# Optimization experiments

Measured on AMD Instinct MI355X. Metric: run time of the kernel, lower is better.

## Reference

```python
import jax, jax.numpy as jnp
import numpy as np

S, N, CM, CZ, H, C = 256, 512, 256, 128, 8, 32
EPS = 1e-5


def layer_norm(x, gamma, beta):
    mu = jnp.mean(x, axis=-1, keepdims=True)
    var = jnp.var(x, axis=-1, keepdims=True)
    return (x - mu) * jax.lax.rsqrt(var + EPS) * gamma + beta


def setup_inputs() -> dict:
    key = jax.random.key(0)
    ks = jax.random.split(key, 10)
    sc = lambda fan_in: 1.0 / np.sqrt(fan_in)
    return {
        "msa_rep": jax.random.normal(ks[0], (S, N, CM), dtype=jnp.float32),
        "pair_rep": jax.random.normal(ks[1], (N, N, CZ), dtype=jnp.float32),
        "ln_msa_g": jnp.ones((CM,), jnp.float32),
        "ln_msa_b": jnp.zeros((CM,), jnp.float32),
        "Wv": jax.random.uniform(ks[2], (CM, H * C), jnp.float32, -sc(CM), sc(CM)),
        "bv": jax.random.uniform(ks[3], (H * C,), jnp.float32, -sc(CM), sc(CM)),
        "ln_z_g": jnp.ones((CZ,), jnp.float32),
        "ln_z_b": jnp.zeros((CZ,), jnp.float32),
        "Wb": jax.random.uniform(ks[4], (CZ, H), jnp.float32, -sc(CZ), sc(CZ)),
        "bb": jax.random.uniform(ks[5], (H,), jnp.float32, -sc(CZ), sc(CZ)),
        "Wg": jax.random.uniform(ks[6], (CM, H * C), jnp.float32, -sc(CM), sc(CM)),
        "bg": jax.random.uniform(ks[7], (H * C,), jnp.float32, -sc(CM), sc(CM)),
        "Wp": jax.random.uniform(ks[8], (H * C, CM), jnp.float32, -sc(H * C), sc(H * C)),
    }


def reference(msa_rep, pair_rep, ln_msa_g, ln_msa_b, Wv, bv, ln_z_g, ln_z_b, Wb, bb, Wg, bg, Wp):
    m = layer_norm(msa_rep, ln_msa_g, ln_msa_b)                 # [S,N,CM]
    v = (m @ Wv + bv).reshape(S, N, H, C)                       # [S,N,H,C]
    g = jax.nn.sigmoid(m @ Wg + bg).reshape(S, N, H, C)         # [S,N,H,C]
    b = layer_norm(pair_rep, ln_z_g, ln_z_b) @ Wb + bb          # [N,N,H]
    w = jax.nn.softmax(b, axis=-2)                              # softmax over key residue j
    # o[s,i,h,c] = sum_j w[i,j,h] * v[s,j,h,c]
    o = g * jnp.einsum('ijh,sjhc->sihc', w, v)                  # [S,N,H,C]
    return o.reshape(S, N, H * C) @ Wp                          # [S,N,CM]
```

## Files before the change

### kernel.cpp

```cpp
#include <hip/hip_runtime.h>
#include <hip/hip_bf16.h>
#include <math.h>

#define S 256
#define N 512
#define CM 256
#define CZ 128
#define H 8
#define C 32
#define HC 256

typedef __attribute__((ext_vector_type(8))) short short8v;
typedef __attribute__((ext_vector_type(4))) float f32x4;

#define GLOBAL_LOAD_LDS16(gsrc, ldst)                                          \
  __builtin_amdgcn_global_load_lds(                                            \
      (const __attribute__((address_space(1))) void*)(gsrc),                   \
      (__attribute__((address_space(3))) void*)(ldst), 16, 0, 0)

__global__ __launch_bounds__(256) void k_prep(
    const float* __restrict__ Wv, const float* __restrict__ Wg, const float* __restrict__ Wp,
    __hip_bfloat16* __restrict__ Wcat_t, __hip_bfloat16* __restrict__ Wp_t)
{
  const int k = blockIdx.x;
  const int n = threadIdx.x;
  Wcat_t[(size_t)n * CM + k]        = __float2bfloat16(Wv[(size_t)k * HC + n]);
  Wcat_t[(size_t)(n + HC) * CM + k] = __float2bfloat16(Wg[(size_t)k * HC + n]);
  Wp_t[(size_t)n * CM + k]          = __float2bfloat16(Wp[(size_t)k * CM + n]);
}

__global__ __launch_bounds__(256) void k_ln(
    const float* __restrict__ msa, const float* __restrict__ gamma, const float* __restrict__ beta,
    __hip_bfloat16* __restrict__ mbf)
{
  const int t = threadIdx.x, wav = t >> 6, lane = t & 63;
  const size_t row = (size_t)blockIdx.x * 4 + wav;
  const int k0 = lane * 4;
  const float4 xv = *(const float4*)(msa + row * CM + k0);
  float s  = xv.x + xv.y + xv.z + xv.w;
  float s2 = xv.x * xv.x + xv.y * xv.y + xv.z * xv.z + xv.w * xv.w;
#pragma unroll
  for (int off = 32; off > 0; off >>= 1) {
    s  += __shfl_xor(s, off);
    s2 += __shfl_xor(s2, off);
  }
  const float mu = s * (1.f / CM);
  const float rstd = rsqrtf(s2 * (1.f / CM) - mu * mu + 1e-5f);
  const float4 gm = *(const float4*)(gamma + k0);
  const float4 bt = *(const float4*)(beta + k0);
  union { __hip_bfloat16 b[4]; short4 v; } pk;
  pk.b[0] = __float2bfloat16((xv.x - mu) * rstd * gm.x + bt.x);
  pk.b[1] = __float2bfloat16((xv.y - mu) * rstd * gm.y + bt.y);
  pk.b[2] = __float2bfloat16((xv.z - mu) * rstd * gm.z + bt.z);
  pk.b[3] = __float2bfloat16((xv.w - mu) * rstd * gm.w + bt.w);
  *(short4*)(mbf + row * CM + k0) = pk.v;
}

__global__ __launch_bounds__(256) void k_mm1(
    const __hip_bfloat16* __restrict__ mbf, const __hip_bfloat16* __restrict__ Wcat_t,
    const float* __restrict__ bv, const float* __restrict__ bg,
    __hip_bfloat16* __restrict__ vc, __hip_bfloat16* __restrict__ gb)
{
  __shared__ __hip_bfloat16 Ac[8 * 128 * 8];
  __shared__ __hip_bfloat16 Bc[8 * 128 * 8];
  const int t = threadIdx.x;
  const int wave = t >> 6, lane = t & 63;
  const int wm = wave >> 1, wn = wave & 1;
  const int lr = lane & 15, lq = lane >> 4;
  const int n0 = blockIdx.x * 128;
  const int m0 = blockIdx.y * 128;

  float bias[4];
#pragma unroll
  for (int ni = 0; ni < 4; ++ni) {
    const int col = n0 + wn * 64 + ni * 16 + lr;
    bias[ni] = (col < HC) ? bv[col] : bg[col - HC];
  }
  f32x4 acc[4][4];
#pragma unroll
  for (int mi = 0; mi < 4; ++mi)
#pragma unroll
    for (int ni = 0; ni < 4; ++ni) acc[mi][ni] = (f32x4)bias[ni];

  for (int kt = 0; kt < CM / 64; ++kt) {
    __syncthreads();
#pragma unroll
    for (int u = 0; u < 2; ++u) {
      const int jb = wave * 2 + u;
#pragma unroll
      for (int ih = 0; ih < 2; ++ih) {
        const __hip_bfloat16* asrc = mbf + ((size_t)(m0 + ih * 64 + lane)) * CM + kt * 64 + jb * 8;
        GLOBAL_LOAD_LDS16(asrc, &Ac[(jb * 128 + ih * 64) * 8]);
        const __hip_bfloat16* bsrc = Wcat_t + ((size_t)(n0 + ih * 64 + lane)) * CM + kt * 64 + jb * 8;
        GLOBAL_LOAD_LDS16(bsrc, &Bc[(jb * 128 + ih * 64) * 8]);
      }
    }
    __syncthreads();
#pragma unroll
    for (int kh = 0; kh < 2; ++kh) {
      const int ldb = lq + kh * 4;
      short8v a[4], b[4];
#pragma unroll
      for (int mi = 0; mi < 4; ++mi)
        a[mi] = *(const short8v*)&Ac[((ldb * 128) + wm * 64 + mi * 16 + lr) * 8];
#pragma unroll
      for (int ni = 0; ni < 4; ++ni)
        b[ni] = *(const short8v*)&Bc[((ldb * 128) + wn * 64 + ni * 16 + lr) * 8];
#pragma unroll
      for (int mi = 0; mi < 4; ++mi)
#pragma unroll
        for (int ni = 0; ni < 4; ++ni)
          acc[mi][ni] = __builtin_amdgcn_mfma_f32_16x16x32_bf16(a[mi], b[ni], acc[mi][ni], 0, 0, 0);
    }
  }

  if (n0 < HC) {
#pragma unroll
    for (int mi = 0; mi < 4; ++mi) {
      const int rowb = m0 + wm * 64 + mi * 16 + lq * 4;
      const int s = rowb >> 9;
      const int j = rowb & (N - 1);
      const int jb = j >> 3, jlo = (lq & 1) * 4;
#pragma unroll
      for (int ni = 0; ni < 4; ++ni) {
        const int col = n0 + wn * 64 + ni * 16 + lr;
        const int h = col >> 5, c = col & 31;
        union { __hip_bfloat16 b[4]; short4 v; } pk;
#pragma unroll
        for (int r = 0; r < 4; ++r) pk.b[r] = __float2bfloat16(acc[mi][ni][r]);
        *(short4*)(vc + ((size_t)(h * (N / 8) + jb) * (S * C) + s * C + c) * 8 + jlo) = pk.v;
      }
    }
  } else {
#pragma unroll
    for (int mi = 0; mi < 4; ++mi) {
      const int rowb = m0 + wm * 64 + mi * 16 + lq * 4;
#pragma unroll
      for (int ni = 0; ni < 4; ++ni) {
        const int colp = (n0 - HC) + wn * 64 + ni * 16 + lr;
#pragma unroll
        for (int r = 0; r < 4; ++r)
          gb[(size_t)(rowb + r) * HC + colp] =
              __float2bfloat16(1.f / (1.f + __expf(-acc[mi][ni][r])));
      }
    }
  }
}

__global__ __launch_bounds__(256) void k_ln_b(
    const float* __restrict__ pair, const float* __restrict__ gamma, const float* __restrict__ beta,
    const float* __restrict__ Wb, float* __restrict__ wbuf)
{
  const int t = threadIdx.x, wav = t >> 6, lane = t & 63;
  const int q = lane & 15, sub = lane >> 4;
  const int k0 = q * 8;

  float wreg[8][8];
#pragma unroll
  for (int kk = 0; kk < 8; ++kk) {
    *(float4*)&wreg[kk][0] = *(const float4*)&Wb[(k0 + kk) * H];
    *(float4*)&wreg[kk][4] = *(const float4*)&Wb[(k0 + kk) * H + 4];
  }
  const float4 gm0 = *(const float4*)(gamma + k0);
  const float4 gm1 = *(const float4*)(gamma + k0 + 4);
  const float4 bt0 = *(const float4*)(beta + k0);
  const float4 bt1 = *(const float4*)(beta + k0 + 4);

#pragma unroll 2
  for (int it = 0; it < 8; ++it) {
    const size_t row = (size_t)blockIdx.x * 128 + it * 16 + wav * 4 + sub;
    const float* x = pair + row * CZ + k0;
    const float4 x0 = *(const float4*)(x);
    const float4 x1 = *(const float4*)(x + 4);

    float s  = x0.x + x0.y + x0.z + x0.w + x1.x + x1.y + x1.z + x1.w;
    float s2 = x0.x * x0.x + x0.y * x0.y + x0.z * x0.z + x0.w * x0.w
             + x1.x * x1.x + x1.y * x1.y + x1.z * x1.z + x1.w * x1.w;
#pragma unroll
    for (int off = 8; off > 0; off >>= 1) {
      s  += __shfl_xor(s, off);
      s2 += __shfl_xor(s2, off);
    }
    const float mu = s * (1.f / CZ);
    const float rstd = rsqrtf(s2 * (1.f / CZ) - mu * mu + 1e-5f);

    float xn[8];
    xn[0] = (x0.x - mu) * rstd * gm0.x + bt0.x;
    xn[1] = (x0.y - mu) * rstd * gm0.y + bt0.y;
    xn[2] = (x0.z - mu) * rstd * gm0.z + bt0.z;
    xn[3] = (x0.w - mu) * rstd * gm0.w + bt0.w;
    xn[4] = (x1.x - mu) * rstd * gm1.x + bt1.x;
    xn[5] = (x1.y - mu) * rstd * gm1.y + bt1.y;
    xn[6] = (x1.z - mu) * rstd * gm1.z + bt1.z;
    xn[7] = (x1.w - mu) * rstd * gm1.w + bt1.w;

    float acc[8];
#pragma unroll
    for (int h = 0; h < 8; ++h) acc[h] = 0.f;
#pragma unroll
    for (int kk = 0; kk < 8; ++kk)
#pragma unroll
      for (int h = 0; h < 8; ++h) acc[h] += xn[kk] * wreg[kk][h];

#pragma unroll
    for (int h = 0; h < 8; ++h) {
#pragma unroll
      for (int off = 8; off > 0; off >>= 1) acc[h] += __shfl_xor(acc[h], off);
    }
    if (q == 0) {
      const size_t i = row >> 9;
      const size_t j = row & (N - 1);
#pragma unroll
      for (int h = 0; h < 8; ++h)
        wbuf[((size_t)h * N + i) * N + j] = acc[h];
    }
  }
}

__global__ __launch_bounds__(256) void k_softmax(
    const float* __restrict__ wbuf, __hip_bfloat16* __restrict__ wbh)
{
  const float* p = wbuf + (size_t)blockIdx.x * N;
  const int t = threadIdx.x, lane = t & 63, wav = t >> 6;
  float2 xv = *(const float2*)(p + t * 2);
  float mx = fmaxf(xv.x, xv.y);
#pragma unroll
  for (int off = 32; off > 0; off >>= 1) mx = fmaxf(mx, __shfl_xor(mx, off));
  __shared__ float redmax[4];
  __shared__ float redsum[4];
  if (lane == 0) redmax[wav] = mx;
  __syncthreads();
  mx = fmaxf(fmaxf(redmax[0], redmax[1]), fmaxf(redmax[2], redmax[3]));
  const float e0 = __expf(xv.x - mx), e1 = __expf(xv.y - mx);
  float sum = e0 + e1;
#pragma unroll
  for (int off = 32; off > 0; off >>= 1) sum += __shfl_xor(sum, off);
  if (lane == 0) redsum[wav] = sum;
  __syncthreads();
  sum = (redsum[0] + redsum[1]) + (redsum[2] + redsum[3]);
  const float inv = 1.f / sum;
  union { __hip_bfloat16 b[2]; int i; } pk;
  pk.b[0] = __float2bfloat16(e0 * inv);
  pk.b[1] = __float2bfloat16(e1 * inv);
  *(int*)((__hip_bfloat16*)(wbh + (size_t)blockIdx.x * N) + t * 2) = pk.i;
}

__global__ __launch_bounds__(256) void k_attn_mfma(
    const __hip_bfloat16* __restrict__ vc, const __hip_bfloat16* __restrict__ wbh,
    __hip_bfloat16* gb)
{
  __shared__ __hip_bfloat16 Ac[8 * 128 * 8];
  __shared__ __hip_bfloat16 Bc[8 * 128 * 8];

  const int t = threadIdx.x;
  const int wave = t >> 6, lane = t & 63;
  const int wm = wave >> 1, wn = wave & 1;
  const int lr = lane & 15, lq = lane >> 4;
  const int n0 = blockIdx.x * 128;
  const int i0 = blockIdx.y * 128;
  const int h  = blockIdx.z;

  f32x4 acc[4][4];
#pragma unroll
  for (int mi = 0; mi < 4; ++mi)
#pragma unroll
    for (int ni = 0; ni < 4; ++ni) acc[mi][ni] = (f32x4)0.f;

  const __hip_bfloat16* Abase = wbh + ((size_t)h * N + i0) * N;
  const __hip_bfloat16* Bbase = vc + (size_t)h * (N / 8) * (S * C) * 8 + (size_t)n0 * 8;

  for (int kt = 0; kt < N / 64; ++kt) {
    __syncthreads();
#pragma unroll
    for (int u = 0; u < 2; ++u) {
      const int jb = wave * 2 + u;
#pragma unroll
      for (int ih = 0; ih < 2; ++ih) {
        const __hip_bfloat16* asrc = Abase + ((size_t)(ih * 64 + lane)) * N + kt * 64 + jb * 8;
        GLOBAL_LOAD_LDS16(asrc, &Ac[(jb * 128 + ih * 64) * 8]);
        const __hip_bfloat16* bsrc = Bbase + ((size_t)(kt * 8 + jb) * (S * C) + ih * 64 + lane) * 8;
        GLOBAL_LOAD_LDS16(bsrc, &Bc[(jb * 128 + ih * 64) * 8]);
      }
    }
    __syncthreads();

#pragma unroll
    for (int kh = 0; kh < 2; ++kh) {
      const int ldb = lq + kh * 4;
      short8v a[4], b[4];
#pragma unroll
      for (int mi = 0; mi < 4; ++mi)
        a[mi] = *(const short8v*)&Ac[((ldb * 128) + wm * 64 + mi * 16 + lr) * 8];
#pragma unroll
      for (int ni = 0; ni < 4; ++ni)
        b[ni] = *(const short8v*)&Bc[((ldb * 128) + wn * 64 + ni * 16 + lr) * 8];
#pragma unroll
      for (int mi = 0; mi < 4; ++mi)
#pragma unroll
        for (int ni = 0; ni < 4; ++ni)
          acc[mi][ni] = __builtin_amdgcn_mfma_f32_16x16x32_bf16(a[mi], b[ni], acc[mi][ni], 0, 0, 0);
    }
  }

#pragma unroll
  for (int mi = 0; mi < 4; ++mi)
#pragma unroll
    for (int ni = 0; ni < 4; ++ni) {
      const int n = n0 + wn * 64 + ni * 16 + lr;
      const int sidx = n >> 5, c = n & 31;
#pragma unroll
      for (int r = 0; r < 4; ++r) {
        const int i = i0 + wm * 64 + mi * 16 + lq * 4 + r;
        const size_t idx = (((size_t)sidx * N + i) << 8) + h * C + c;
        const float gv = __bfloat162float(gb[idx]);
        gb[idx] = __float2bfloat16(gv * acc[mi][ni][r]);
      }
    }
}

__global__ __launch_bounds__(256) void k_out_mfma(
    const __hip_bfloat16* __restrict__ ogb, const __hip_bfloat16* __restrict__ Wp_t,
    float* __restrict__ out)
{
  __shared__ __hip_bfloat16 Ac[8 * 128 * 8];
  __shared__ __hip_bfloat16 Bc[8 * 128 * 8];
  const int t = threadIdx.x;
  const int wave = t >> 6, lane = t & 63;
  const int wm = wave >> 1, wn = wave & 1;
  const int lr = lane & 15, lq = lane >> 4;
  const int n0 = blockIdx.x * 128;
  const int m0 = blockIdx.y * 128;

  f32x4 acc[4][4];
#pragma unroll
  for (int mi = 0; mi < 4; ++mi)
#pragma unroll
    for (int ni = 0; ni < 4; ++ni) acc[mi][ni] = (f32x4)0.f;

  for (int kt = 0; kt < CM / 64; ++kt) {
    __syncthreads();
#pragma unroll
    for (int u = 0; u < 2; ++u) {
      const int jb = wave * 2 + u;
#pragma unroll
      for (int ih = 0; ih < 2; ++ih) {
        const __hip_bfloat16* asrc = ogb + ((size_t)(m0 + ih * 64 + lane)) * CM + kt * 64 + jb * 8;
        GLOBAL_LOAD_LDS16(asrc, &Ac[(jb * 128 + ih * 64) * 8]);
        const __hip_bfloat16* bsrc = Wp_t + ((size_t)(n0 + ih * 64 + lane)) * CM + kt * 64 + jb * 8;
        GLOBAL_LOAD_LDS16(bsrc, &Bc[(jb * 128 + ih * 64) * 8]);
      }
    }
    __syncthreads();
#pragma unroll
    for (int kh = 0; kh < 2; ++kh) {
      const int ldb = lq + kh * 4;
      short8v a[4], b[4];
#pragma unroll
      for (int mi = 0; mi < 4; ++mi)
        a[mi] = *(const short8v*)&Ac[((ldb * 128) + wm * 64 + mi * 16 + lr) * 8];
#pragma unroll
      for (int ni = 0; ni < 4; ++ni)
        b[ni] = *(const short8v*)&Bc[((ldb * 128) + wn * 64 + ni * 16 + lr) * 8];
#pragma unroll
      for (int mi = 0; mi < 4; ++mi)
#pragma unroll
        for (int ni = 0; ni < 4; ++ni)
          acc[mi][ni] = __builtin_amdgcn_mfma_f32_16x16x32_bf16(a[mi], b[ni], acc[mi][ni], 0, 0, 0);
    }
  }

#pragma unroll
  for (int mi = 0; mi < 4; ++mi) {
    const int rowb = m0 + wm * 64 + mi * 16 + lq * 4;
#pragma unroll
    for (int ni = 0; ni < 4; ++ni) {
      const int col = n0 + wn * 64 + ni * 16 + lr;
#pragma unroll
      for (int r = 0; r < 4; ++r)
        out[(size_t)(rowb + r) * CM + col] = acc[mi][ni][r];
    }
  }
}

extern "C" void kernel_launch(void* const* d_in, const int* in_sizes, int n_in,
                              void* d_out, int out_size, void* d_ws, size_t ws_size,
                              hipStream_t stream)
{
  const float* msa      = (const float*)d_in[0];
  const float* pair     = (const float*)d_in[1];
  const float* ln_msa_g = (const float*)d_in[2];
  const float* ln_msa_b = (const float*)d_in[3];
  const float* Wv       = (const float*)d_in[4];
  const float* bv       = (const float*)d_in[5];
  const float* ln_z_g   = (const float*)d_in[6];
  const float* ln_z_b   = (const float*)d_in[7];
  const float* Wb       = (const float*)d_in[8];
  const float* bb       = (const float*)d_in[9];
  const float* Wg       = (const float*)d_in[10];
  const float* bg       = (const float*)d_in[11];
  const float* Wp       = (const float*)d_in[12];
  float* out = (float*)d_out;
  (void)bb;

  char* w = (char*)d_ws;
  __hip_bfloat16* vc     = (__hip_bfloat16*)(w);
  __hip_bfloat16* mbf    = (__hip_bfloat16*)(w + 67108864);
  __hip_bfloat16* gb     = (__hip_bfloat16*)(w + 134217728);
  float*          wbuf   = (float*)         (w + 201326592);
  __hip_bfloat16* wbh    = (__hip_bfloat16*)(w + 209715200);
  __hip_bfloat16* Wcat_t = (__hip_bfloat16*)(w + 213909504);
  __hip_bfloat16* Wp_t   = (__hip_bfloat16*)(w + 214171648);

  k_prep<<<256, 256, 0, stream>>>(Wv, Wg, Wp, Wcat_t, Wp_t);
  k_ln<<<S * N / 4, 256, 0, stream>>>(msa, ln_msa_g, ln_msa_b, mbf);
  dim3 g1(4, S * N / 128);
  k_mm1<<<g1, 256, 0, stream>>>(mbf, Wcat_t, bv, bg, vc, gb);
  k_ln_b<<<N * N / 128, 256, 0, stream>>>(pair, ln_z_g, ln_z_b, Wb, wbuf);
  k_softmax<<<N * H, 256, 0, stream>>>(wbuf, wbh);
  dim3 g4(S * C / 128, N / 128, H);
  k_attn_mfma<<<g4, 256, 0, stream>>>(vc, wbh, gb);
  dim3 g5(2, S * N / 128);
  k_out_mfma<<<g5, 256, 0, stream>>>(gb, Wp_t, out);
}
```

Baseline: 331.3 us.

## Double-buffer LDS staging in GEMM kernels and transpose MFMA outputs for vector stores

Adds two-stage LDS double buffering to the mm1, attention and output GEMMs, so the next K-tile's global-to-LDS loads are issued before the current tile's MFMAs run. This uses one barrier per iteration instead of two. In the gate half of mm1 and in the attention kernel, the MFMA operands are swapped so each lane holds 4 contiguous columns, which lets the epilogue write packed short4 stores and read-modify-write gb in 4-element chunks instead of scattered 2-byte accesses. The attention grid is reordered so blocks sharing the same V columns (n0) run adjacently, which may improve L2 reuse. LDS usage doubles to 64KB per block, which may reduce occupancy.

```diff
diff --git a/kernel.cpp b/kernel.cpp
--- a/kernel.cpp
+++ b/kernel.cpp
@@ -61,60 +61,83 @@
     const float* __restrict__ bv, const float* __restrict__ bg,
     __hip_bfloat16* __restrict__ vc, __hip_bfloat16* __restrict__ gb)
 {
-  __shared__ __hip_bfloat16 Ac[8 * 128 * 8];
-  __shared__ __hip_bfloat16 Bc[8 * 128 * 8];
+  __shared__ __hip_bfloat16 Ac[2][8 * 128 * 8];
+  __shared__ __hip_bfloat16 Bc[2][8 * 128 * 8];
   const int t = threadIdx.x;
   const int wave = t >> 6, lane = t & 63;
   const int wm = wave >> 1, wn = wave & 1;
   const int lr = lane & 15, lq = lane >> 4;
   const int n0 = blockIdx.x * 128;
   const int m0 = blockIdx.y * 128;
-
-  float bias[4];
-#pragma unroll
-  for (int ni = 0; ni < 4; ++ni) {
-    const int col = n0 + wn * 64 + ni * 16 + lr;
-    bias[ni] = (col < HC) ? bv[col] : bg[col - HC];
-  }
+  const bool vhalf = (n0 < HC);
+
   f32x4 acc[4][4];
-#pragma unroll
-  for (int mi = 0; mi < 4; ++mi)
-#pragma unroll
-    for (int ni = 0; ni < 4; ++ni) acc[mi][ni] = (f32x4)bias[ni];
-
-  for (int kt = 0; kt < CM / 64; ++kt) {
-    __syncthreads();
+  if (vhalf) {
+#pragma unroll
+    for (int ni = 0; ni < 4; ++ni) {
+      const float b_ = bv[n0 + wn * 64 + ni * 16 + lr];
+#pragma unroll
+      for (int mi = 0; mi < 4; ++mi) acc[mi][ni] = (f32x4)b_;
+    }
+  } else {
+#pragma unroll
+    for (int ni = 0; ni < 4; ++ni) {
+      const float4 b4 = *(const float4*)&bg[(n0 - HC) + wn * 64 + ni * 16 + lq * 4];
+#pragma unroll
+      for (int mi = 0; mi < 4; ++mi) {
+        acc[mi][ni][0] = b4.x; acc[mi][ni][1] = b4.y;
+        acc[mi][ni][2] = b4.z; acc[mi][ni][3] = b4.w;
+      }
+    }
+  }
+
+  auto stage = [&](int p, int kt) {
 #pragma unroll
     for (int u = 0; u < 2; ++u) {
       const int jb = wave * 2 + u;
 #pragma unroll
       for (int ih = 0; ih < 2; ++ih) {
-        const __hip_bfloat16* asrc = mbf + ((size_t)(m0 + ih * 64 + lane)) * CM + kt * 64 + jb * 8;
-        GLOBAL_LOAD_LDS16(asrc, &Ac[(jb * 128 + ih * 64) * 8]);
-        const __hip_bfloat16* bsrc = Wcat_t + ((size_t)(n0 + ih * 64 + lane)) * CM + kt * 64 + jb * 8;
-        GLOBAL_LOAD_LDS16(bsrc, &Bc[(jb * 128 + ih * 64) * 8]);
-      }
-    }
-    __syncthreads();
+        GLOBAL_LOAD_LDS16(mbf + ((size_t)(m0 + ih * 64 + lane)) * CM + kt * 64 + jb * 8,
+                          &Ac[p][(jb * 128 + ih * 64) * 8]);
+        GLOBAL_LOAD_LDS16(Wcat_t + ((size_t)(n0 + ih * 64 + lane)) * CM + kt * 64 + jb * 8,
+                          &Bc[p][(jb * 128 + ih * 64) * 8]);
+      }
+    }
+  };
+
+  stage(0, 0);
+  __syncthreads();
+  for (int kt = 0; kt < 4; ++kt) {
+    const int p = kt & 1;
+    if (kt < 3) stage(p ^ 1, kt + 1);
 #pragma unroll
     for (int kh = 0; kh < 2; ++kh) {
       const int ldb = lq + kh * 4;
       short8v a[4], b[4];
 #pragma unroll
       for (int mi = 0; mi < 4; ++mi)
-        a[mi] = *(const short8v*)&Ac[((ldb * 128) + wm * 64 + mi * 16 + lr) * 8];
+        a[mi] = *(const short8v*)&Ac[p][((ldb * 128) + wm * 64 + mi * 16 + lr) * 8];
 #pragma unroll
       for (int ni = 0; ni < 4; ++ni)
-        b[ni] = *(const short8v*)&Bc[((ldb * 128) + wn * 64 + ni * 16 + lr) * 8];
-#pragma unroll
-      for (int mi = 0; mi < 4; ++mi)
-#pragma unroll
-        for (int ni = 0; ni < 4; ++ni)
-          acc[mi][ni] = __builtin_amdgcn_mfma_f32_16x16x32_bf16(a[mi], b[ni], acc[mi][ni], 0, 0, 0);
-    }
-  }
-
-  if (n0 < HC) {
+        b[ni] = *(const short8v*)&Bc[p][((ldb * 128) + wn * 64 + ni * 16 + lr) * 8];
+      if (vhalf) {
+#pragma unroll
+        for (int mi = 0; mi < 4; ++mi)
+#pragma unroll
+          for (int ni = 0; ni < 4; ++ni)
+            acc[mi][ni] = __builtin_amdgcn_mfma_f32_16x16x32_bf16(a[mi], b[ni], acc[mi][ni], 0, 0, 0);
+      } else {
+#pragma unroll
+        for (int mi = 0; mi < 4; ++mi)
+#pragma unroll
+          for (int ni = 0; ni < 4; ++ni)
+            acc[mi][ni] = __builtin_amdgcn_mfma_f32_16x16x32_bf16(b[ni], a[mi], acc[mi][ni], 0, 0, 0);
+      }
+    }
+    __syncthreads();
+  }
+
+  if (vhalf) {
 #pragma unroll
     for (int mi = 0; mi < 4; ++mi) {
       const int rowb = m0 + wm * 64 + mi * 16 + lq * 4;
@@ -134,14 +157,15 @@
   } else {
 #pragma unroll
     for (int mi = 0; mi < 4; ++mi) {
-      const int rowb = m0 + wm * 64 + mi * 16 + lq * 4;
+      const int rowb = m0 + wm * 64 + mi * 16 + lr;
 #pragma unroll
       for (int ni = 0; ni < 4; ++ni) {
-        const int colp = (n0 - HC) + wn * 64 + ni * 16 + lr;
+        const int nb = (n0 - HC) + wn * 64 + ni * 16 + lq * 4;
+        union { __hip_bfloat16 b[4]; short4 v; } pk;
 #pragma unroll
         for (int r = 0; r < 4; ++r)
-          gb[(size_t)(rowb + r) * HC + colp] =
-              __float2bfloat16(1.f / (1.f + __expf(-acc[mi][ni][r])));
+          pk.b[r] = __float2bfloat16(1.f / (1.f + __expf(-acc[mi][ni][r])));
+        *(short4*)(gb + (size_t)rowb * HC + nb) = pk.v;
       }
     }
   }
@@ -249,15 +273,15 @@
     const __hip_bfloat16* __restrict__ vc, const __hip_bfloat16* __restrict__ wbh,
     __hip_bfloat16* gb)
 {
-  __shared__ __hip_bfloat16 Ac[8 * 128 * 8];
-  __shared__ __hip_bfloat16 Bc[8 * 128 * 8];
+  __shared__ __hip_bfloat16 Ac[2][8 * 128 * 8];
+  __shared__ __hip_bfloat16 Bc[2][8 * 128 * 8];
 
   const int t = threadIdx.x;
   const int wave = t >> 6, lane = t & 63;
   const int wm = wave >> 1, wn = wave & 1;
   const int lr = lane & 15, lq = lane >> 4;
-  const int n0 = blockIdx.x * 128;
-  const int i0 = blockIdx.y * 128;
+  const int i0 = blockIdx.x * 128;
+  const int n0 = blockIdx.y * 128;
   const int h  = blockIdx.z;
 
   f32x4 acc[4][4];
@@ -269,61 +293,68 @@
   const __hip_bfloat16* Abase = wbh + ((size_t)h * N + i0) * N;
   const __hip_bfloat16* Bbase = vc + (size_t)h * (N / 8) * (S * C) * 8 + (size_t)n0 * 8;
 
-  for (int kt = 0; kt < N / 64; ++kt) {
-    __syncthreads();
+  auto stage = [&](int p, int kt) {
 #pragma unroll
     for (int u = 0; u < 2; ++u) {
       const int jb = wave * 2 + u;
 #pragma unroll
       for (int ih = 0; ih < 2; ++ih) {
-        const __hip_bfloat16* asrc = Abase + ((size_t)(ih * 64 + lane)) * N + kt * 64 + jb * 8;
-        GLOBAL_LOAD_LDS16(asrc, &Ac[(jb * 128 + ih * 64) * 8]);
-        const __hip_bfloat16* bsrc = Bbase + ((size_t)(kt * 8 + jb) * (S * C) + ih * 64 + lane) * 8;
-        GLOBAL_LOAD_LDS16(bsrc, &Bc[(jb * 128 + ih * 64) * 8]);
-      }
-    }
-    __syncthreads();
-
+        GLOBAL_LOAD_LDS16(Abase + ((size_t)(ih * 64 + lane)) * N + kt * 64 + jb * 8,
+                          &Ac[p][(jb * 128 + ih * 64) * 8]);
+        GLOBAL_LOAD_LDS16(Bbase + ((size_t)(kt * 8 + jb) * (S * C) + ih * 64 + lane) * 8,
+                          &Bc[p][(jb * 128 + ih * 64) * 8]);
+      }
+    }
+  };
+
+  stage(0, 0);
+  __syncthreads();
+  for (int kt = 0; kt < 8; ++kt) {
+    const int p = kt & 1;
+    if (kt < 7) stage(p ^ 1, kt + 1);
 #pragma unroll
     for (int kh = 0; kh < 2; ++kh) {
       const int ldb = lq + kh * 4;
       short8v a[4], b[4];
 #pragma unroll
       for (int mi = 0; mi < 4; ++mi)
-        a[mi] = *(const short8v*)&Ac[((ldb * 128) + wm * 64 + mi * 16 + lr) * 8];
+        a[mi] = *(const short8v*)&Ac[p][((ldb * 128) + wm * 64 + mi * 16 + lr) * 8];
 #pragma unroll
       for (int ni = 0; ni < 4; ++ni)
-        b[ni] = *(const short8v*)&Bc[((ldb * 128) + wn * 64 + ni * 16 + lr) * 8];
+        b[ni] = *(const short8v*)&Bc[p][((ldb * 128) + wn * 64 + ni * 16 + lr) * 8];
 #pragma unroll
       for (int mi = 0; mi < 4; ++mi)
 #pragma unroll
         for (int ni = 0; ni < 4; ++ni)
-          acc[mi][ni] = __builtin_amdgcn_mfma_f32_16x16x32_bf16(a[mi], b[ni], acc[mi][ni], 0, 0, 0);
-    }
-  }
-
-#pragma unroll
-  for (int mi = 0; mi < 4; ++mi)
+          acc[mi][ni] = __builtin_amdgcn_mfma_f32_16x16x32_bf16(b[ni], a[mi], acc[mi][ni], 0, 0, 0);
+    }
+    __syncthreads();
+  }
+
+#pragma unroll
+  for (int mi = 0; mi < 4; ++mi) {
+    const int i = i0 + wm * 64 + mi * 16 + lr;
 #pragma unroll
     for (int ni = 0; ni < 4; ++ni) {
-      const int n = n0 + wn * 64 + ni * 16 + lr;
-      const int sidx = n >> 5, c = n & 31;
-#pragma unroll
-      for (int r = 0; r < 4; ++r) {
-        const int i = i0 + wm * 64 + mi * 16 + lq * 4 + r;
-        const size_t idx = (((size_t)sidx * N + i) << 8) + h * C + c;
-        const float gv = __bfloat162float(gb[idx]);
-        gb[idx] = __float2bfloat16(gv * acc[mi][ni][r]);
-      }
-    }
+      const int nb = n0 + wn * 64 + ni * 16 + lq * 4;
+      const int sidx = nb >> 5, c = nb & 31;
+      __hip_bfloat16* gp = gb + (((size_t)sidx * N + i) << 8) + h * C + c;
+      union { __hip_bfloat16 b[4]; short4 v; } gl, st;
+      gl.v = *(const short4*)gp;
+#pragma unroll
+      for (int r = 0; r < 4; ++r)
+        st.b[r] = __float2bfloat16(__bfloat162float(gl.b[r]) * acc[mi][ni][r]);
+      *(short4*)gp = st.v;
+    }
+  }
 }
 
 __global__ __launch_bounds__(256) void k_out_mfma(
     const __hip_bfloat16* __restrict__ ogb, const __hip_bfloat16* __restrict__ Wp_t,
     float* __restrict__ out)
 {
-  __shared__ __hip_bfloat16 Ac[8 * 128 * 8];
-  __shared__ __hip_bfloat16 Bc[8 * 128 * 8];
+  __shared__ __hip_bfloat16 Ac[2][8 * 128 * 8];
+  __shared__ __hip_bfloat16 Bc[2][8 * 128 * 8];
   const int t = threadIdx.x;
   const int wave = t >> 6, lane = t & 63;
   const int wm = wave >> 1, wn = wave & 1;
@@ -337,36 +368,42 @@
 #pragma unroll
     for (int ni = 0; ni < 4; ++ni) acc[mi][ni] = (f32x4)0.f;
 
-  for (int kt = 0; kt < CM / 64; ++kt) {
-    __syncthreads();
+  auto stage = [&](int p, int kt) {
 #pragma unroll
     for (int u = 0; u < 2; ++u) {
       const int jb = wave * 2 + u;
 #pragma unroll
       for (int ih = 0; ih < 2; ++ih) {
-        const __hip_bfloat16* asrc = ogb + ((size_t)(m0 + ih * 64 + lane)) * CM + kt * 64 + jb * 8;
-        GLOBAL_LOAD_LDS16(asrc, &Ac[(jb * 128 + ih * 64) * 8]);
-        const __hip_bfloat16* bsrc = Wp_t + ((size_t)(n0 + ih * 64 + lane)) * CM + kt * 64 + jb * 8;
-        GLOBAL_LOAD_LDS16(bsrc, &Bc[(jb * 128 + ih * 64) * 8]);
-      }
-    }
-    __syncthreads();
+        GLOBAL_LOAD_LDS16(ogb + ((size_t)(m0 + ih * 64 + lane)) * CM + kt * 64 + jb * 8,
+                          &Ac[p][(jb * 128 + ih * 64) * 8]);
+        GLOBAL_LOAD_LDS16(Wp_t + ((size_t)(n0 + ih * 64 + lane)) * CM + kt * 64 + jb * 8,
+                          &Bc[p][(jb * 128 + ih * 64) * 8]);
+      }
+    }
+  };
+
+  stage(0, 0);
+  __syncthreads();
+  for (int kt = 0; kt < 4; ++kt) {
+    const int p = kt & 1;
+    if (kt < 3) stage(p ^ 1, kt + 1);
 #pragma unroll
     for (int kh = 0; kh < 2; ++kh) {
       const int ldb = lq + kh * 4;
       short8v a[4], b[4];
 #pragma unroll
       for (int mi = 0; mi < 4; ++mi)
-        a[mi] = *(const short8v*)&Ac[((ldb * 128) + wm * 64 + mi * 16 + lr) * 8];
+        a[mi] = *(const short8v*)&Ac[p][((ldb * 128) + wm * 64 + mi * 16 + lr) * 8];
 #pragma unroll
       for (int ni = 0; ni < 4; ++ni)
-        b[ni] = *(const short8v*)&Bc[((ldb * 128) + wn * 64 + ni * 16 + lr) * 8];
+        b[ni] = *(const short8v*)&Bc[p][((ldb * 128) + wn * 64 + ni * 16 + lr) * 8];
 #pragma unroll
       for (int mi = 0; mi < 4; ++mi)
 #pragma unroll
         for (int ni = 0; ni < 4; ++ni)
           acc[mi][ni] = __builtin_amdgcn_mfma_f32_16x16x32_bf16(a[mi], b[ni], acc[mi][ni], 0, 0, 0);
     }
+    __syncthreads();
   }
 
 #pragma unroll
@@ -417,7 +454,7 @@
   k_mm1<<<g1, 256, 0, stream>>>(mbf, Wcat_t, bv, bg, vc, gb);
   k_ln_b<<<N * N / 128, 256, 0, stream>>>(pair, ln_z_g, ln_z_b, Wb, wbuf);
   k_softmax<<<N * H, 256, 0, stream>>>(wbuf, wbh);
-  dim3 g4(S * C / 128, N / 128, H);
+  dim3 g4(4, S * C / 128, H);
   k_attn_mfma<<<g4, 256, 0, stream>>>(vc, wbh, gb);
   dim3 g5(2, S * N / 128);
   k_out_mfma<<<g5, 256, 0, stream>>>(gb, Wp_t, out);
```

Measured after the change: 363.0 us. +9.6%, slower.

## Enlarge GEMM tiles to 256 rows with 8 waves; fuse pair LN-bias with softmax

Applied to the files above, without the earlier changes.

The three MFMA GEMM kernels move to 512-thread blocks covering 256 M rows, so each B tile loaded into LDS is reused by twice as many rows and the grid has half as many blocks. Separately, the pair layernorm/bias projection and the softmax are fused into one kernel per query row i. The logits stay in shared memory instead of making a float round trip through global memory, and one kernel launch is removed. In exchange the larger LDS footprint and register use per block may lower occupancy, and the fused kernel runs only N=512 blocks.

```diff
diff --git a/kernel.cpp b/kernel.cpp
--- a/kernel.cpp
+++ b/kernel.cpp
@@ -56,25 +56,26 @@
   *(short4*)(mbf + row * CM + k0) = pk.v;
 }
 
-__global__ __launch_bounds__(256) void k_mm1(
+__global__ __launch_bounds__(512) void k_mm1(
     const __hip_bfloat16* __restrict__ mbf, const __hip_bfloat16* __restrict__ Wcat_t,
     const float* __restrict__ bv, const float* __restrict__ bg,
     __hip_bfloat16* __restrict__ vc, __hip_bfloat16* __restrict__ gb)
 {
-  __shared__ __hip_bfloat16 Ac[8 * 128 * 8];
+  __shared__ __hip_bfloat16 Ac[8 * 256 * 8];
   __shared__ __hip_bfloat16 Bc[8 * 128 * 8];
   const int t = threadIdx.x;
   const int wave = t >> 6, lane = t & 63;
   const int wm = wave >> 1, wn = wave & 1;
   const int lr = lane & 15, lq = lane >> 4;
   const int n0 = blockIdx.x * 128;
-  const int m0 = blockIdx.y * 128;
+  const int m0 = blockIdx.y * 256;
+  const bool vhalf = (n0 < HC);
 
   float bias[4];
 #pragma unroll
   for (int ni = 0; ni < 4; ++ni) {
     const int col = n0 + wn * 64 + ni * 16 + lr;
-    bias[ni] = (col < HC) ? bv[col] : bg[col - HC];
+    bias[ni] = vhalf ? bv[col] : bg[col - HC];
   }
   f32x4 acc[4][4];
 #pragma unroll
@@ -85,15 +86,18 @@
   for (int kt = 0; kt < CM / 64; ++kt) {
     __syncthreads();
 #pragma unroll
+    for (int u = 0; u < 4; ++u) {
+      const int cc = wave * 4 + u;
+      const int kb = cc & 7, ih = cc >> 3;
+      GLOBAL_LOAD_LDS16(mbf + ((size_t)(m0 + ih * 64 + lane)) * CM + kt * 64 + kb * 8,
+                        &Ac[(kb * 256 + ih * 64 + lane) * 8]);
+    }
+#pragma unroll
     for (int u = 0; u < 2; ++u) {
-      const int jb = wave * 2 + u;
-#pragma unroll
-      for (int ih = 0; ih < 2; ++ih) {
-        const __hip_bfloat16* asrc = mbf + ((size_t)(m0 + ih * 64 + lane)) * CM + kt * 64 + jb * 8;
-        GLOBAL_LOAD_LDS16(asrc, &Ac[(jb * 128 + ih * 64) * 8]);
-        const __hip_bfloat16* bsrc = Wcat_t + ((size_t)(n0 + ih * 64 + lane)) * CM + kt * 64 + jb * 8;
-        GLOBAL_LOAD_LDS16(bsrc, &Bc[(jb * 128 + ih * 64) * 8]);
-      }
+      const int cc = wave * 2 + u;
+      const int kb = cc & 7, ih = cc >> 3;
+      GLOBAL_LOAD_LDS16(Wcat_t + ((size_t)(n0 + ih * 64 + lane)) * CM + kt * 64 + kb * 8,
+                        &Bc[(kb * 128 + ih * 64 + lane) * 8]);
     }
     __syncthreads();
 #pragma unroll
@@ -102,7 +106,7 @@
       short8v a[4], b[4];
 #pragma unroll
       for (int mi = 0; mi < 4; ++mi)
-        a[mi] = *(const short8v*)&Ac[((ldb * 128) + wm * 64 + mi * 16 + lr) * 8];
+        a[mi] = *(const short8v*)&Ac[((ldb * 256) + wm * 64 + mi * 16 + lr) * 8];
 #pragma unroll
       for (int ni = 0; ni < 4; ++ni)
         b[ni] = *(const short8v*)&Bc[((ldb * 128) + wn * 64 + ni * 16 + lr) * 8];
@@ -114,7 +118,7 @@
     }
   }
 
-  if (n0 < HC) {
+  if (vhalf) {
 #pragma unroll
     for (int mi = 0; mi < 4; ++mi) {
       const int rowb = m0 + wm * 64 + mi * 16 + lq * 4;
@@ -147,13 +151,15 @@
   }
 }
 
-__global__ __launch_bounds__(256) void k_ln_b(
+__global__ __launch_bounds__(256) void k_lnb_sm(
     const float* __restrict__ pair, const float* __restrict__ gamma, const float* __restrict__ beta,
-    const float* __restrict__ Wb, float* __restrict__ wbuf)
-{
+    const float* __restrict__ Wb, __hip_bfloat16* __restrict__ wbh)
+{
+  __shared__ float slog[H][N];
   const int t = threadIdx.x, wav = t >> 6, lane = t & 63;
   const int q = lane & 15, sub = lane >> 4;
   const int k0 = q * 8;
+  const size_t i = blockIdx.x;
 
   float wreg[8][8];
 #pragma unroll
@@ -167,9 +173,9 @@
   const float4 bt1 = *(const float4*)(beta + k0 + 4);
 
 #pragma unroll 2
-  for (int it = 0; it < 8; ++it) {
-    const size_t row = (size_t)blockIdx.x * 128 + it * 16 + wav * 4 + sub;
-    const float* x = pair + row * CZ + k0;
+  for (int it = 0; it < 32; ++it) {
+    const int j = it * 16 + wav * 4 + sub;
+    const float* x = pair + (i * N + j) * CZ + k0;
     const float4 x0 = *(const float4*)(x);
     const float4 x1 = *(const float4*)(x + 4);
 
@@ -208,48 +214,43 @@
       for (int off = 8; off > 0; off >>= 1) acc[h] += __shfl_xor(acc[h], off);
     }
     if (q == 0) {
-      const size_t i = row >> 9;
-      const size_t j = row & (N - 1);
-#pragma unroll
-      for (int h = 0; h < 8; ++h)
-        wbuf[((size_t)h * N + i) * N + j] = acc[h];
-    }
-  }
-}
-
-__global__ __launch_bounds__(256) void k_softmax(
-    const float* __restrict__ wbuf, __hip_bfloat16* __restrict__ wbh)
-{
-  const float* p = wbuf + (size_t)blockIdx.x * N;
-  const int t = threadIdx.x, lane = t & 63, wav = t >> 6;
-  float2 xv = *(const float2*)(p + t * 2);
-  float mx = fmaxf(xv.x, xv.y);
-#pragma unroll
-  for (int off = 32; off > 0; off >>= 1) mx = fmaxf(mx, __shfl_xor(mx, off));
-  __shared__ float redmax[4];
-  __shared__ float redsum[4];
-  if (lane == 0) redmax[wav] = mx;
+#pragma unroll
+      for (int h = 0; h < 8; ++h) slog[h][j] = acc[h];
+    }
+  }
   __syncthreads();
-  mx = fmaxf(fmaxf(redmax[0], redmax[1]), fmaxf(redmax[2], redmax[3]));
-  const float e0 = __expf(xv.x - mx), e1 = __expf(xv.y - mx);
-  float sum = e0 + e1;
-#pragma unroll
-  for (int off = 32; off > 0; off >>= 1) sum += __shfl_xor(sum, off);
-  if (lane == 0) redsum[wav] = sum;
-  __syncthreads();
-  sum = (redsum[0] + redsum[1]) + (redsum[2] + redsum[3]);
-  const float inv = 1.f / sum;
-  union { __hip_bfloat16 b[2]; int i; } pk;
-  pk.b[0] = __float2bfloat16(e0 * inv);
-  pk.b[1] = __float2bfloat16(e1 * inv);
-  *(int*)((__hip_bfloat16*)(wbh + (size_t)blockIdx.x * N) + t * 2) = pk.i;
-}
-
-__global__ __launch_bounds__(256) void k_attn_mfma(
+
+#pragma unroll
+  for (int hh2 = 0; hh2 < 2; ++hh2) {
+    const int hh = wav * 2 + hh2;
+    const int j0 = lane * 8;
+    const float4 p0 = *(const float4*)&slog[hh][j0];
+    const float4 p1 = *(const float4*)&slog[hh][j0 + 4];
+    float mx = fmaxf(fmaxf(fmaxf(p0.x, p0.y), fmaxf(p0.z, p0.w)),
+                     fmaxf(fmaxf(p1.x, p1.y), fmaxf(p1.z, p1.w)));
+#pragma unroll
+    for (int off = 32; off > 0; off >>= 1) mx = fmaxf(mx, __shfl_xor(mx, off));
+    float e[8];
+    e[0] = __expf(p0.x - mx); e[1] = __expf(p0.y - mx);
+    e[2] = __expf(p0.z - mx); e[3] = __expf(p0.w - mx);
+    e[4] = __expf(p1.x - mx); e[5] = __expf(p1.y - mx);
+    e[6] = __expf(p1.z - mx); e[7] = __expf(p1.w - mx);
+    float sum = ((e[0] + e[1]) + (e[2] + e[3])) + ((e[4] + e[5]) + (e[6] + e[7]));
+#pragma unroll
+    for (int off = 32; off > 0; off >>= 1) sum += __shfl_xor(sum, off);
+    const float inv = 1.f / sum;
+    union { __hip_bfloat16 b[8]; short8v v; } pk;
+#pragma unroll
+    for (int r = 0; r < 8; ++r) pk.b[r] = __float2bfloat16(e[r] * inv);
+    *(short8v*)(wbh + ((size_t)hh * N + i) * N + j0) = pk.v;
+  }
+}
+
+__global__ __launch_bounds__(512) void k_attn_mfma(
     const __hip_bfloat16* __restrict__ vc, const __hip_bfloat16* __restrict__ wbh,
     __hip_bfloat16* gb)
 {
-  __shared__ __hip_bfloat16 Ac[8 * 128 * 8];
+  __shared__ __hip_bfloat16 Ac[8 * 256 * 8];
   __shared__ __hip_bfloat16 Bc[8 * 128 * 8];
 
   const int t = threadIdx.x;
@@ -257,7 +258,7 @@
   const int wm = wave >> 1, wn = wave & 1;
   const int lr = lane & 15, lq = lane >> 4;
   const int n0 = blockIdx.x * 128;
-  const int i0 = blockIdx.y * 128;
+  const int i0 = blockIdx.y * 256;
   const int h  = blockIdx.z;
 
   f32x4 acc[4][4];
@@ -272,15 +273,18 @@
   for (int kt = 0; kt < N / 64; ++kt) {
     __syncthreads();
 #pragma unroll
+    for (int u = 0; u < 4; ++u) {
+      const int cc = wave * 4 + u;
+      const int kb = cc & 7, ih = cc >> 3;
+      GLOBAL_LOAD_LDS16(Abase + ((size_t)(ih * 64 + lane)) * N + kt * 64 + kb * 8,
+                        &Ac[(kb * 256 + ih * 64 + lane) * 8]);
+    }
+#pragma unroll
     for (int u = 0; u < 2; ++u) {
-      const int jb = wave * 2 + u;
-#pragma unroll
-      for (int ih = 0; ih < 2; ++ih) {
-        const __hip_bfloat16* asrc = Abase + ((size_t)(ih * 64 + lane)) * N + kt * 64 + jb * 8;
-        GLOBAL_LOAD_LDS16(asrc, &Ac[(jb * 128 + ih * 64) * 8]);
-        const __hip_bfloat16* bsrc = Bbase + ((size_t)(kt * 8 + jb) * (S * C) + ih * 64 + lane) * 8;
-        GLOBAL_LOAD_LDS16(bsrc, &Bc[(jb * 128 + ih * 64) * 8]);
-      }
+      const int cc = wave * 2 + u;
+      const int kb = cc & 7, ih = cc >> 3;
+      GLOBAL_LOAD_LDS16(Bbase + ((size_t)(kt * 8 + kb) * (S * C) + ih * 64 + lane) * 8,
+                        &Bc[(kb * 128 + ih * 64 + lane) * 8]);
     }
     __syncthreads();
 
@@ -290,7 +294,7 @@
       short8v a[4], b[4];
 #pragma unroll
       for (int mi = 0; mi < 4; ++mi)
-        a[mi] = *(const short8v*)&Ac[((ldb * 128) + wm * 64 + mi * 16 + lr) * 8];
+        a[mi] = *(const short8v*)&Ac[((ldb * 256) + wm * 64 + mi * 16 + lr) * 8];
 #pragma unroll
       for (int ni = 0; ni < 4; ++ni)
         b[ni] = *(const short8v*)&Bc[((ldb * 128) + wn * 64 + ni * 16 + lr) * 8];
@@ -318,18 +322,18 @@
     }
 }
 
-__global__ __launch_bounds__(256) void k_out_mfma(
+__global__ __launch_bounds__(512) void k_out_mfma(
     const __hip_bfloat16* __restrict__ ogb, const __hip_bfloat16* __restrict__ Wp_t,
     float* __restrict__ out)
 {
-  __shared__ __hip_bfloat16 Ac[8 * 128 * 8];
+  __shared__ __hip_bfloat16 Ac[8 * 256 * 8];
   __shared__ __hip_bfloat16 Bc[8 * 128 * 8];
   const int t = threadIdx.x;
   const int wave = t >> 6, lane = t & 63;
   const int wm = wave >> 1, wn = wave & 1;
   const int lr = lane & 15, lq = lane >> 4;
   const int n0 = blockIdx.x * 128;
-  const int m0 = blockIdx.y * 128;
+  const int m0 = blockIdx.y * 256;
 
   f32x4 acc[4][4];
 #pragma unroll
@@ -340,15 +344,18 @@
   for (int kt = 0; kt < CM / 64; ++kt) {
     __syncthreads();
 #pragma unroll
+    for (int u = 0; u < 4; ++u) {
+      const int cc = wave * 4 + u;
+      const int kb = cc & 7, ih = cc >> 3;
+      GLOBAL_LOAD_LDS16(ogb + ((size_t)(m0 + ih * 64 + lane)) * CM + kt * 64 + kb * 8,
+                        &Ac[(kb * 256 + ih * 64 + lane) * 8]);
+    }
+#pragma unroll
     for (int u = 0; u < 2; ++u) {
-      const int jb = wave * 2 + u;
-#pragma unroll
-      for (int ih = 0; ih < 2; ++ih) {
-        const __hip_bfloat16* asrc = ogb + ((size_t)(m0 + ih * 64 + lane)) * CM + kt * 64 + jb * 8;
-        GLOBAL_LOAD_LDS16(asrc, &Ac[(jb * 128 + ih * 64) * 8]);
-        const __hip_bfloat16* bsrc = Wp_t + ((size_t)(n0 + ih * 64 + lane)) * CM + kt * 64 + jb * 8;
-        GLOBAL_LOAD_LDS16(bsrc, &Bc[(jb * 128 + ih * 64) * 8]);
-      }
+      const int cc = wave * 2 + u;
+      const int kb = cc & 7, ih = cc >> 3;
+      GLOBAL_LOAD_LDS16(Wp_t + ((size_t)(n0 + ih * 64 + lane)) * CM + kt * 64 + kb * 8,
+                        &Bc[(kb * 128 + ih * 64 + lane) * 8]);
     }
     __syncthreads();
 #pragma unroll
@@ -357,7 +364,7 @@
       short8v a[4], b[4];
 #pragma unroll
       for (int mi = 0; mi < 4; ++mi)
-        a[mi] = *(const short8v*)&Ac[((ldb * 128) + wm * 64 + mi * 16 + lr) * 8];
+        a[mi] = *(const short8v*)&Ac[((ldb * 256) + wm * 64 + mi * 16 + lr) * 8];
 #pragma unroll
       for (int ni = 0; ni < 4; ++ni)
         b[ni] = *(const short8v*)&Bc[((ldb * 128) + wn * 64 + ni * 16 + lr) * 8];
@@ -406,19 +413,17 @@
   __hip_bfloat16* vc     = (__hip_bfloat16*)(w);
   __hip_bfloat16* mbf    = (__hip_bfloat16*)(w + 67108864);
   __hip_bfloat16* gb     = (__hip_bfloat16*)(w + 134217728);
-  float*          wbuf   = (float*)         (w + 201326592);
   __hip_bfloat16* wbh    = (__hip_bfloat16*)(w + 209715200);
   __hip_bfloat16* Wcat_t = (__hip_bfloat16*)(w + 213909504);
   __hip_bfloat16* Wp_t   = (__hip_bfloat16*)(w + 214171648);
 
   k_prep<<<256, 256, 0, stream>>>(Wv, Wg, Wp, Wcat_t, Wp_t);
   k_ln<<<S * N / 4, 256, 0, stream>>>(msa, ln_msa_g, ln_msa_b, mbf);
-  dim3 g1(4, S * N / 128);
-  k_mm1<<<g1, 256, 0, stream>>>(mbf, Wcat_t, bv, bg, vc, gb);
-  k_ln_b<<<N * N / 128, 256, 0, stream>>>(pair, ln_z_g, ln_z_b, Wb, wbuf);
-  k_softmax<<<N * H, 256, 0, stream>>>(wbuf, wbh);
-  dim3 g4(S * C / 128, N / 128, H);
-  k_attn_mfma<<<g4, 256, 0, stream>>>(vc, wbh, gb);
-  dim3 g5(2, S * N / 128);
-  k_out_mfma<<<g5, 256, 0, stream>>>(gb, Wp_t, out);
-}
+  dim3 g1(4, S * N / 256);
+  k_mm1<<<g1, 512, 0, stream>>>(mbf, Wcat_t, bv, bg, vc, gb);
+  k_lnb_sm<<<N, 256, 0, stream>>>(pair, ln_z_g, ln_z_b, Wb, wbh);
+  dim3 g4(S * C / 128, N / 256, H);
+  k_attn_mfma<<<g4, 512, 0, stream>>>(vc, wbh, gb);
+  dim3 g5(2, S * N / 256);
+  k_out_mfma<<<g5, 512, 0, stream>>>(gb, Wp_t, out);
+}
```

New measurement: 329.5 us. No clear change (-0.5%).
